# Optimization experiments

Measured on AMD Instinct MI355X. Metric: run time of the kernel, lower is better.

The kernel has to match this reference:

```python
import jax, jax.numpy as jnp
import numpy as np
from jax.scipy.special import logsumexp

LOG2PI = float(np.log(2.0 * np.pi))
N_GRID = 25  # dim == 2 -> N = 25
NEG = -1e9


def _cond_logprob(cand, hist_loc, hist_t, t, beta, sigma):
    # cand [B,M,d], hist_loc [B,H,d], hist_t [B,H], t [B]
    d = cand.shape[-1]
    logw = -beta * (t[:, None] - hist_t)                       # [B,H]
    logw = logw - logsumexp(logw, axis=1, keepdims=True)
    diff = cand[:, :, None, :] - hist_loc[:, None, :, :]       # [B,M,H,d]
    sq = jnp.sum(diff * diff, axis=-1)                         # [B,M,H]
    logN = -0.5 * sq / (sigma * sigma) - d * jnp.log(sigma) - 0.5 * d * LOG2PI
    return logsumexp(logw[:, None, :] + logN, axis=-1)         # [B,M]


def _gmm_call(times, locs, beta, sigma):
    # causal GMM loglik: event k explained by mixture over events j<k
    B, L, d = locs.shape
    dt = times[:, :, None] - times[:, None, :]                 # [B,L,L]
    mask = jnp.tril(jnp.ones((L, L), dtype=bool), -1)          # j < k
    raw = jnp.where(mask, -beta * dt, NEG)
    logw = raw - logsumexp(raw, axis=-1, keepdims=True)
    diff = locs[:, :, None, :] - locs[:, None, :, :]           # [B,L,L,d]
    sq = jnp.sum(diff * diff, axis=-1)
    logN = -0.5 * sq / (sigma * sigma) - d * jnp.log(sigma) - 0.5 * d * LOG2PI
    logp = logsumexp(jnp.where(mask, logw + logN, NEG), axis=-1)  # [B,L]
    logp0 = -0.5 * jnp.sum(locs[:, 0] ** 2, axis=-1) - 0.5 * d * LOG2PI
    return logp0 + jnp.sum(logp[:, 1:], axis=-1)               # [B]


def setup_inputs() -> dict:
    key = jax.random.key(0)
    ks = jax.random.split(key, 6)
    B, H, PLTS, D = 64, 384, 16, 2
    input_time = jnp.sort(jax.random.uniform(ks[0], (B, H), dtype=jnp.float32), axis=1)
    curr_time = 1.0 + jnp.sort(jax.random.uniform(ks[1], (B, PLTS), dtype=jnp.float32), axis=1)
    history_data = jax.random.normal(ks[2], (B, H, D), dtype=jnp.float32)
    expected_data = jax.random.normal(ks[3], (B, PLTS, D), dtype=jnp.float32)
    aux_state_in = jax.random.normal(ks[4], (B, H, 1), dtype=jnp.float32)
    aux_state_out = jax.random.normal(ks[5], (B, PLTS, 1), dtype=jnp.float32)
    beta = jnp.ones((1,), dtype=jnp.float32)
    log_sigma = jnp.zeros((1,), dtype=jnp.float32)
    return {"curr_time": curr_time, "input_time": input_time,
            "history_data": history_data, "expected_data": expected_data,
            "aux_state_in": aux_state_in, "aux_state_out": aux_state_out,
            "beta": beta, "log_sigma": log_sigma}


def reference(curr_time, input_time, history_data, expected_data,
              aux_state_in, aux_state_out, beta, log_sigma):
    sigma = jnp.exp(log_sigma)
    B, plts, d = expected_data.shape
    hist = history_data
    times = input_time
    preds = []
    for i in range(plts):
        expected_loc = expected_data[:, i, :]                  # [B,d]
        nd = jnp.concatenate([hist, expected_loc[:, None, :]], axis=1)  # [B,H+1,d]
        # faithful to source: bounds from event rows 0 and 1 (scalar min/max)
        minx, maxx = jnp.min(nd[:, 0]), jnp.max(nd[:, 0])
        miny, maxy = jnp.min(nd[:, 1]), jnp.max(nd[:, 1])
        xlim = jnp.linspace(minx, maxx, N_GRID)
        ylim = jnp.linspace(miny, maxy, N_GRID)
        X1, X2 = jnp.meshgrid(xlim, ylim)
        arr = jnp.stack([X1.reshape(-1), X2.reshape(-1)], axis=1)  # [N*N,2]
        cand = jnp.broadcast_to(arr[None], (B, N_GRID * N_GRID, 2))
        ll = _cond_logprob(cand, hist, times, curr_time[:, i], beta, sigma)  # [B,N*N]
        arg = jnp.argmin(ll, axis=-1)                          # [B]
        predicted = jnp.take_along_axis(cand, arg[:, None, None], axis=1)[:, 0, :]  # [B,2]
        preds.append(predicted)
        hist = jnp.concatenate([hist, predicted[:, None, :]], axis=1)
        times = jnp.concatenate([times, curr_time[:, i:i + 1]], axis=1)
    spatial_loglik = _gmm_call(times, hist, beta, sigma)       # [B]
    predicted_out = jnp.stack(preds, axis=0)                   # [plts,B,2]
    return spatial_loglik, predicted_out
```

## Files before the change

### kernel.cpp

```cpp
#include <hip/hip_runtime.h>
#include <hip/hip_bf16.h>
#include <math.h>

#define BB    64
#define HH    384
#define PLTS  16
#define LMAX  (HH + PLTS)
#define NG    25
#define NC    (NG * NG)
#define BLOCK 1024
#define NWAVES (BLOCK / 64)
#define NUNIT (3 * NC)

#if defined(__has_builtin) && __has_builtin(__builtin_amdgcn_exp2f)
static __device__ __forceinline__ float fast_exp2(float x) { return __builtin_amdgcn_exp2f(x); }
#else
static __device__ __forceinline__ float fast_exp2(float x) { return exp2f(x); }
#endif
#if defined(__has_builtin) && __has_builtin(__builtin_amdgcn_logf)
static __device__ __forceinline__ float fast_log2(float x) { return __builtin_amdgcn_logf(x); }
#else
static __device__ __forceinline__ float fast_log2(float x) { return log2f(x); }
#endif

__global__ __launch_bounds__(BLOCK)
void spatio_kernel(const float* __restrict__ ct,
                   const float* __restrict__ it,
                   const float* __restrict__ hd,
                   const float* __restrict__ beta_p,
                   const float* __restrict__ lsig_p,
                   float* __restrict__ out)
{
    __shared__ __align__(16) float u_s [LMAX];
    __shared__ __align__(16) float px_s[LMAX];
    __shared__ __align__(16) float py_s[LMAX];
    __shared__ float  w2s[LMAX];
    __shared__ float2 hxy[LMAX];
    __shared__ float  Pscan[NUNIT];
    __shared__ float  Pg[BLOCK];
    __shared__ float  rowt[16];
    __shared__ float  pre[LMAX];
    __shared__ float  wsum[NWAVES];
    __shared__ float  rv[NWAVES];
    __shared__ float  sb[4];

    const int b    = blockIdx.x;
    const int tid  = threadIdx.x;
    const int lane = tid & 63;
    const int wave = tid >> 6;

    const float LOG2E  = 1.4426950408889634f;
    const float LN2    = 0.69314718055994531f;
    const float LOG2PI = 1.8378770664093453f;
    const float INF    = __builtin_inff();

    const float beta  = beta_p[0];
    const float lsig  = lsig_p[0];
    const float sigma = fast_exp2(lsig * LOG2E);
    const float cc    = -0.5f / (sigma * sigma);
    const float c2    = cc * LOG2E;
    const float bl    = beta * LOG2E;
    const float Sc    = -2.0f * lsig - LOG2PI;

    for (int j = tid; j < HH; j += BLOCK) {
        float t = it[b * HH + j];
        float x = hd[(b * HH + j) * 2 + 0];
        float y = hd[(b * HH + j) * 2 + 1];
        float w = bl * t;
        w2s[j]  = w;
        hxy[j]  = make_float2(x, y);
        u_s[j]  = fmaf(c2, x * x + y * y, w);
        px_s[j] = -2.0f * c2 * x;
        py_s[j] = -2.0f * c2 * y;
    }

    float wn_r[16];
    if (wave == 0) {
        const float4* ct4 = (const float4*)(ct + b * PLTS);
        float4 c0 = ct4[0], c1 = ct4[1], c2v = ct4[2], c3 = ct4[3];
        wn_r[0]=bl*c0.x;  wn_r[1]=bl*c0.y;  wn_r[2]=bl*c0.z;  wn_r[3]=bl*c0.w;
        wn_r[4]=bl*c1.x;  wn_r[5]=bl*c1.y;  wn_r[6]=bl*c1.z;  wn_r[7]=bl*c1.w;
        wn_r[8]=bl*c2v.x; wn_r[9]=bl*c2v.y; wn_r[10]=bl*c2v.z;wn_r[11]=bl*c2v.w;
        wn_r[12]=bl*c3.x; wn_r[13]=bl*c3.y; wn_r[14]=bl*c3.z; wn_r[15]=bl*c3.w;
    } else {
        #pragma unroll
        for (int k = 0; k < 16; ++k) wn_r[k] = 0.0f;
    }

    if (tid < 64) {
        const float* p = hd + tid * (HH * 2);
        float p0x = p[0], p0y = p[1], p1x = p[2], p1y = p[3];
        float xmn = fminf(p0x, p0y), xmx = fmaxf(p0x, p0y);
        float ymn = fminf(p1x, p1y), ymx = fmaxf(p1x, p1y);
        for (int o = 32; o > 0; o >>= 1) {
            xmn = fminf(xmn, __shfl_down(xmn, o, 64));
            xmx = fmaxf(xmx, __shfl_down(xmx, o, 64));
            ymn = fminf(ymn, __shfl_down(ymn, o, 64));
            ymx = fmaxf(ymx, __shfl_down(ymx, o, 64));
        }
        if (tid == 0) { sb[0] = xmn; sb[1] = xmx; sb[2] = ymn; sb[3] = ymx; }
    }
    __syncthreads();

    const float minx = sb[0], maxx = sb[1], miny = sb[2], maxy = sb[3];
    const float stepx = (maxx - minx) * (1.0f / 24.0f);
    const float stepy = (maxy - miny) * (1.0f / 24.0f);

    {
        const float4* u4  = (const float4*)u_s;
        const float4* px4 = (const float4*)px_s;
        const float4* py4 = (const float4*)py_s;
        #pragma unroll
        for (int rep = 0; rep < 2; ++rep) {
            int u = tid + rep * BLOCK;
            if (u < NUNIT) {
                int cand = u % NC;
                int part = u / NC;
                int kx = cand % NG, ky = cand / NG;
                float cx = fmaf((float)kx, stepx, minx);
                float cy = fmaf((float)ky, stepy, miny);
                float Ac = c2 * (cx * cx + cy * cy);
                int g0 = part * 32;
                float s0 = 0.f, s1 = 0.f, s2 = 0.f, s3 = 0.f;
                #pragma unroll 8
                for (int g = g0; g < g0 + 32; ++g) {
                    float4 U = u4[g], PX = px4[g], PY = py4[g];
                    s0 += fast_exp2(fmaf(PX.x, cx, fmaf(PY.x, cy, U.x + Ac)));
                    s1 += fast_exp2(fmaf(PX.y, cx, fmaf(PY.y, cy, U.y + Ac)));
                    s2 += fast_exp2(fmaf(PX.z, cx, fmaf(PY.z, cy, U.z + Ac)));
                    s3 += fast_exp2(fmaf(PX.w, cx, fmaf(PY.w, cy, U.w + Ac)));
                }
                Pscan[u] = (s0 + s1) + (s2 + s3);
            }
        }
    }
    __syncthreads();

    if (wave == 0) {
        float Sv[10], cxk[10], cyk[10];
        const int cbase = lane * 10;
        #pragma unroll
        for (int k = 0; k < 10; ++k) {
            int c = cbase + k;
            if (c < NC) {
                Sv[k] = Pscan[c] + Pscan[c + NC] + Pscan[c + 2 * NC];
                int ky = (int)((c + 0.5f) * 0.04f);
                int kx = c - 25 * ky;
                cxk[k] = fmaf((float)kx, stepx, minx);
                cyk[k] = fmaf((float)ky, stepy, miny);
            } else {
                Sv[k] = INF; cxk[k] = 0.0f; cyk[k] = 0.0f;
            }
        }
        #pragma unroll
        for (int i = 0; i < PLTS; ++i) {
            float v = Sv[0]; int ik = 0;
            #pragma unroll
            for (int k = 1; k < 10; ++k)
                if (Sv[k] < v) { v = Sv[k]; ik = k; }
            int idx = cbase + ik;
            #pragma unroll
            for (int o = 1; o < 64; o <<= 1) {
                float ov = __shfl_xor(v, o, 64);
                int   oi = __shfl_xor(idx, o, 64);
                if (ov < v || (ov == v && oi < idx)) { v = ov; idx = oi; }
            }
            int   ky = (int)((idx + 0.5f) * 0.04f);
            int   kx = idx - 25 * ky;
            float px = fmaf((float)kx, stepx, minx);
            float py = fmaf((float)ky, stepy, miny);
            float wn = wn_r[i];
            if (lane == 0) {
                const int L = HH + i;
                w2s[L]  = wn;
                hxy[L]  = make_float2(px, py);
                u_s[L]  = fmaf(c2, px * px + py * py, wn);
                px_s[L] = -2.0f * c2 * px;
                py_s[L] = -2.0f * c2 * py;
                out[BB + (i * BB + b) * 2 + 0] = px;
                out[BB + (i * BB + b) * 2 + 1] = py;
            }
            #pragma unroll
            for (int k = 0; k < 10; ++k) {
                float dx = px - cxk[k], dy = py - cyk[k];
                Sv[k] += fast_exp2(fmaf(c2, fmaf(dx, dx, dy * dy), wn));
            }
        }
    } else {
        const int t2 = tid - 64;
        int row = 0, c = 0;
        if (t2 < 100)      { row = t2 + 1; c = 0; }
        else if (t2 < 300) { int u = t2 - 100; row = 101 + (u >> 1); c = u & 1; }
        else if (t2 < 600) { int u = t2 - 300; int q = u / 3; row = 201 + q; c = u - 3 * q; }
        else if (t2 < 932) { int u = t2 - 600; row = 301 + (u >> 2); c = u & 3; }
        float part = 0.0f;
        if (row > 0) {
            int j0 = c * 100;
            int j1 = min(row, j0 + 100);
            float2 hi = hxy[row];
            float xi = hi.x, yi = hi.y;
            float Ai = c2 * fmaf(xi, xi, yi * yi);
            float a0 = 0.f, a1 = 0.f;
            int j = j0;
            for (; j + 1 < j1; j += 2) {
                a0 += fast_exp2(fmaf(px_s[j],     xi, fmaf(py_s[j],     yi, u_s[j]     + Ai)));
                a1 += fast_exp2(fmaf(px_s[j + 1], xi, fmaf(py_s[j + 1], yi, u_s[j + 1] + Ai)));
            }
            if (j < j1)
                a0 += fast_exp2(fmaf(px_s[j], xi, fmaf(py_s[j], yi, u_s[j] + Ai)));
            part = a0 + a1;
        }
        Pg[tid] = part;
    }
    __syncthreads();

    {
        const int row = HH + wave;
        int j0 = lane * 7;
        int j1 = min(row, j0 + 7);
        float2 hi = hxy[row];
        float xi = hi.x, yi = hi.y;
        float Ai = c2 * fmaf(xi, xi, yi * yi);
        float part = 0.0f;
        for (int j = j0; j < j1; ++j)
            part += fast_exp2(fmaf(px_s[j], xi, fmaf(py_s[j], yi, u_s[j] + Ai)));
        for (int o = 32; o > 0; o >>= 1) part += __shfl_down(part, o, 64);
        if (lane == 0) rowt[wave] = part;
    }

    float x = (tid < LMAX) ? fast_exp2(w2s[tid]) : 0.0f;
    for (int o = 1; o < 64; o <<= 1) {
        float y = __shfl_up(x, o, 64);
        if (lane >= o) x += y;
    }
    if (lane == 63) wsum[wave] = x;
    __syncthreads();
    float off = 0.0f;
    for (int w = 0; w < wave; ++w) off += wsum[w];
    if (tid < LMAX) pre[tid] = x + off;
    __syncthreads();

    float acc = 0.0f;
    if (tid >= 1 && tid < LMAX) {
        const int row = tid;
        float tot;
        if (row <= 100)      { tot = Pg[64 + row - 1]; }
        else if (row <= 200) { int base = 64 + 100 + (row - 101) * 2;
                               tot = Pg[base] + Pg[base + 1]; }
        else if (row <= 300) { int base = 64 + 300 + (row - 201) * 3;
                               tot = Pg[base] + Pg[base + 1] + Pg[base + 2]; }
        else if (row <= 383) { int base = 64 + 600 + (row - 301) * 4;
                               tot = (Pg[base] + Pg[base + 1]) + (Pg[base + 2] + Pg[base + 3]); }
        else                 { tot = rowt[row - HH]; }
        acc = Sc + LN2 * (fast_log2(tot) - fast_log2(pre[row - 1]));
    }
    for (int o = 32; o > 0; o >>= 1) acc += __shfl_down(acc, o, 64);
    if (lane == 0) rv[wave] = acc;
    __syncthreads();
    if (tid == 0) {
        float tot = 0.0f;
        for (int w = 0; w < NWAVES; ++w) tot += rv[w];
        float2 h0 = hxy[0];
        tot += -0.5f * (h0.x * h0.x + h0.y * h0.y) - LOG2PI;
        out[b] = tot;
    }
}

extern "C" void kernel_launch(void* const* d_in, const int* in_sizes, int n_in,
                              void* d_out, int out_size, void* d_ws, size_t ws_size,
                              hipStream_t stream) {
    const float* ct   = (const float*)d_in[0];
    const float* it   = (const float*)d_in[1];
    const float* hd   = (const float*)d_in[2];
    const float* beta = (const float*)d_in[6];
    const float* lsig = (const float*)d_in[7];
    float* out = (float*)d_out;

    hipLaunchKernelGGL(spatio_kernel, dim3(BB), dim3(BLOCK), 0, stream,
                       ct, it, hd, beta, lsig, out);
}
```

Baseline: 94.23 us.

## Factor grid Gaussian into separable x/y exponent tables and dot products

Uses the separability of the 2D Gaussian on a regular grid: it precomputes per-row x-factor (with the weight folded in) and per-column y-factor exponent tables in shared memory, 25x384 each. The per-candidate sum then becomes a dot product of two table rows instead of one exp2 per candidate-history pair. This cuts exp evaluations from about 625x384 to 2x25x384 and replaces them with FMAs, and the split drops from three parts to two. The cost is about 78KB of extra LDS, an extra barrier, and the risk of underflow when the two factors are computed separately.

```diff
diff --git a/kernel.cpp b/kernel.cpp
--- a/kernel.cpp
+++ b/kernel.cpp
@@ -10,7 +10,9 @@
 #define NC    (NG * NG)
 #define BLOCK 1024
 #define NWAVES (BLOCK / 64)
-#define NUNIT (3 * NC)
+#define FSTR  388
+#define KHALF 192
+#define NUNIT (2 * NC)
 
 #if defined(__has_builtin) && __has_builtin(__builtin_amdgcn_exp2f)
 static __device__ __forceinline__ float fast_exp2(float x) { return __builtin_amdgcn_exp2f(x); }
@@ -31,12 +33,14 @@
                    const float* __restrict__ lsig_p,
                    float* __restrict__ out)
 {
+    __shared__ __align__(16) float FxT[NG][FSTR];
+    __shared__ __align__(16) float FyT[NG][FSTR];
     __shared__ __align__(16) float u_s [LMAX];
     __shared__ __align__(16) float px_s[LMAX];
     __shared__ __align__(16) float py_s[LMAX];
     __shared__ float  w2s[LMAX];
     __shared__ float2 hxy[LMAX];
-    __shared__ float  Pscan[NUNIT];
+    __shared__ float  P[NUNIT];
     __shared__ float  Pg[BLOCK];
     __shared__ float  rowt[16];
     __shared__ float  pre[LMAX];
@@ -106,32 +110,40 @@
     const float stepx = (maxx - minx) * (1.0f / 24.0f);
     const float stepy = (maxy - miny) * (1.0f / 24.0f);
 
-    {
-        const float4* u4  = (const float4*)u_s;
-        const float4* px4 = (const float4*)px_s;
-        const float4* py4 = (const float4*)py_s;
-        #pragma unroll
-        for (int rep = 0; rep < 2; ++rep) {
-            int u = tid + rep * BLOCK;
-            if (u < NUNIT) {
-                int cand = u % NC;
-                int part = u / NC;
-                int kx = cand % NG, ky = cand / NG;
-                float cx = fmaf((float)kx, stepx, minx);
-                float cy = fmaf((float)ky, stepy, miny);
-                float Ac = c2 * (cx * cx + cy * cy);
-                int g0 = part * 32;
-                float s0 = 0.f, s1 = 0.f, s2 = 0.f, s3 = 0.f;
-                #pragma unroll 8
-                for (int g = g0; g < g0 + 32; ++g) {
-                    float4 U = u4[g], PX = px4[g], PY = py4[g];
-                    s0 += fast_exp2(fmaf(PX.x, cx, fmaf(PY.x, cy, U.x + Ac)));
-                    s1 += fast_exp2(fmaf(PX.y, cx, fmaf(PY.y, cy, U.y + Ac)));
-                    s2 += fast_exp2(fmaf(PX.z, cx, fmaf(PY.z, cy, U.z + Ac)));
-                    s3 += fast_exp2(fmaf(PX.w, cx, fmaf(PY.w, cy, U.w + Ac)));
-                }
-                Pscan[u] = (s0 + s1) + (s2 + s3);
-            }
+    for (int idx = tid; idx < NG * HH; idx += BLOCK) {
+        int row = idx / HH;
+        int j   = idx - row * HH;
+        float2 h = hxy[j];
+        float cxr = fmaf((float)row, stepx, minx);
+        float cyr = fmaf((float)row, stepy, miny);
+        float dx = cxr - h.x;
+        float dy = cyr - h.y;
+        FxT[row][j] = fast_exp2(fmaf(c2 * dx, dx, w2s[j]));
+        FyT[row][j] = fast_exp2(c2 * dy * dy);
+    }
+    __syncthreads();
+
+    #pragma unroll
+    for (int rep = 0; rep < 2; ++rep) {
+        int u = tid + rep * BLOCK;
+        if (u < NUNIT) {
+            int h    = (u >= NC) ? 1 : 0;
+            int c    = u - h * NC;
+            int ky   = c / NG;
+            int kx   = c - NG * ky;
+            const float4* fx4 = (const float4*)&FxT[kx][0];
+            const float4* fy4 = (const float4*)&FyT[ky][0];
+            int g0 = h * (KHALF / 4);
+            float s0 = 0.f, s1 = 0.f, s2 = 0.f, s3 = 0.f;
+            #pragma unroll 8
+            for (int g = g0; g < g0 + KHALF / 4; ++g) {
+                float4 a = fx4[g], bv = fy4[g];
+                s0 = fmaf(a.x, bv.x, s0);
+                s1 = fmaf(a.y, bv.y, s1);
+                s2 = fmaf(a.z, bv.z, s2);
+                s3 = fmaf(a.w, bv.w, s3);
+            }
+            P[u] = (s0 + s1) + (s2 + s3);
         }
     }
     __syncthreads();
@@ -143,7 +155,7 @@
         for (int k = 0; k < 10; ++k) {
             int c = cbase + k;
             if (c < NC) {
-                Sv[k] = Pscan[c] + Pscan[c + NC] + Pscan[c + 2 * NC];
+                Sv[k] = P[c] + P[c + NC];
                 int ky = (int)((c + 0.5f) * 0.04f);
                 int kx = c - 25 * ky;
                 cxk[k] = fmaf((float)kx, stepx, minx);
```

Result: faster. 89.31 us (-5.2%).
